# Kernel tuning notes

Hardware: AMD Instinct MI355X
Metric: run time of the kernel (lower is better)

The kernel has to match this reference:

```python
import jax, jax.numpy as jnp
import numpy as np

INF = 1e30
B, L, D_IN, D_STATE, HIDDEN = 32, 4096, 150, 75, 75


def setup_inputs() -> dict:
    key = jax.random.key(0)
    k_in, k_st, k_m, k_w0, k_b0, k_w1, k_b1 = jax.random.split(key, 7)
    inputs = jax.random.normal(k_in, (B, L, D_IN), dtype=jnp.float32)
    state = jax.random.normal(k_st, (B, D_STATE), dtype=jnp.float32)
    c_mask = jax.random.randint(k_m, (B, L), 0, 2).astype(bool)
    # Linear params; torch nn.Linear init scale ~ 1/sqrt(fan_in)
    W0 = jax.random.normal(k_w0, (D_STATE + D_IN, HIDDEN), dtype=jnp.float32) / np.sqrt(D_STATE + D_IN)
    b0 = jax.random.normal(k_b0, (HIDDEN,), dtype=jnp.float32) / np.sqrt(D_STATE + D_IN)
    W1 = jax.random.normal(k_w1, (HIDDEN, 1), dtype=jnp.float32) / np.sqrt(HIDDEN)
    b1 = jax.random.normal(k_b1, (1,), dtype=jnp.float32) / np.sqrt(HIDDEN)
    return {"inputs": inputs, "state": state, "c_mask": c_mask,
            "W0": W0, "b0": b0, "W1": W1, "b1": b1}


def reference(inputs, state, c_mask, W0, b0, W1, b1):
    b, l, _ = inputs.shape
    # u: [B, L, D_STATE + D_IN]  (state broadcast along L, concat with inputs)
    u = jnp.concatenate(
        [jnp.broadcast_to(state[:, None, :], (b, l, state.shape[-1])), inputs],
        axis=2)
    s0 = jnp.tanh(u @ W0 + b0)               # [B, L, HIDDEN]
    s = (s0 @ W1 + b1)[..., 0]               # [B, L]
    s1 = s - INF * (1.0 - c_mask.astype(s.dtype))
    a = jax.nn.softmax(s1, axis=-1)           # [B, L]
    res = jnp.sum(inputs * a[..., None], axis=1, keepdims=True)  # [B, 1, D_IN]
    return res, s1
```

## Files before the change

### kernel.cpp

```cpp
#include <hip/hip_runtime.h>

#define B_    32
#define L_    4096
#define DIN   150
#define DST   75
#define HID   75
#define HPAD  80
#define INF30 1e30f
#define SPART 152


__device__ __forceinline__ float tanh_fast(float p) {
    float e = __expf(-2.f * fabsf(p));
    float t = (1.f - e) / (1.f + e);
    return copysignf(t, p);
}

__global__ __launch_bounds__(256) void k_prep(
    const float* __restrict__ W0, const float* __restrict__ W1,
    float* __restrict__ W0p, float* __restrict__ W1p) {
    int i = blockIdx.x * 256 + threadIdx.x;
    if (i < DIN * HPAD) {
        int d = i / HPAD, h = i - d * HPAD;
        W0p[i] = (h < HID) ? W0[(DST + d) * HID + h] : 0.f;
    }
    if (i < HPAD) W1p[i] = (i < HID) ? W1[i] : 0.f;
}

__global__ __launch_bounds__(128) void k_statepre(
    const float* __restrict__ state, const float* __restrict__ W0,
    const float* __restrict__ b0, float* __restrict__ sp) {
    int b = blockIdx.x;
    int h = threadIdx.x;
    if (h < HPAD) {
        float acc = 0.f;
        if (h < HID) {
            acc = b0[h];
            #pragma unroll 5
            for (int k = 0; k < DST; ++k)
                acc = fmaf(state[b * DST + k], W0[k * HID + h], acc);
        }
        sp[b * HPAD + h] = acc;
    }
}

__global__ __launch_bounds__(256, 4) void k_main(
    const float* __restrict__ in, const unsigned char* __restrict__ maskB,
    const float* __restrict__ W0p, const float* __restrict__ W1p,
    const float* __restrict__ b1, const float* __restrict__ sp,
    float* __restrict__ s1out, float* __restrict__ part) {
    __shared__ __align__(16) float XT[DIN * 64];
    __shared__ __align__(16) float sred2[4 * 64];
    __shared__ __align__(16) float wvals[64];

    int blk = blockIdx.x, tid = threadIdx.x;
    int b = blk >> 6, l0 = (blk & 63) << 6;
    const float4* src4 = (const float4*)(in + (size_t)(b * L_ + l0) * DIN);

    #pragma unroll
    for (int p = 0; p < 10; ++p) {
        int i4 = p * 256 + tid;
        if (i4 < 2400) {
            float4 v = src4[i4];
            int idx = i4 << 2;
            float vals[4] = {v.x, v.y, v.z, v.w};
            #pragma unroll
            for (int e = 0; e < 4; ++e) {
                int id = idx + e;
                int r = id / DIN;
                int k = id - r * DIN;
                XT[(k << 6) + (((r >> 2) ^ (k & 15)) << 2) + (r & 3)] = vals[e];
            }
        }
    }
    __syncthreads();

    int rg = tid & 15, cg = tid >> 4;
    float acc[4][5];
    {
        float s0 = sp[b * HPAD + (cg << 2) + 0];
        float s1_ = sp[b * HPAD + (cg << 2) + 1];
        float s2 = sp[b * HPAD + (cg << 2) + 2];
        float s3 = sp[b * HPAD + (cg << 2) + 3];
        float s4 = sp[b * HPAD + 64 + cg];
        #pragma unroll
        for (int j = 0; j < 4; ++j) {
            acc[j][0] = s0; acc[j][1] = s1_; acc[j][2] = s2;
            acc[j][3] = s3; acc[j][4] = s4;
        }
    }
    const float* wb4 = W0p + (cg << 2);
    const float* wb1 = W0p + 64 + cg;
    #pragma unroll 6
    for (int k = 0; k < DIN; ++k) {
        float4 xv = *(const float4*)&XT[(k << 6) + ((rg ^ (k & 15)) << 2)];
        float4 wv = *(const float4*)&wb4[k * HPAD];
        float  w4 = wb1[k * HPAD];
        float xj[4] = {xv.x, xv.y, xv.z, xv.w};
        #pragma unroll
        for (int j = 0; j < 4; ++j) {
            acc[j][0] = fmaf(xj[j], wv.x, acc[j][0]);
            acc[j][1] = fmaf(xj[j], wv.y, acc[j][1]);
            acc[j][2] = fmaf(xj[j], wv.z, acc[j][2]);
            acc[j][3] = fmaf(xj[j], wv.w, acc[j][3]);
            acc[j][4] = fmaf(xj[j], w4,   acc[j][4]);
        }
    }

    float w1a = W1p[(cg << 2) + 0], w1b = W1p[(cg << 2) + 1];
    float w1c = W1p[(cg << 2) + 2], w1d = W1p[(cg << 2) + 3];
    float w1e = W1p[64 + cg];
    int wv_ = tid >> 6, lane = tid & 63;
    float spart[4];
    #pragma unroll
    for (int j = 0; j < 4; ++j) {
        float s = 0.f;
        s = fmaf(tanh_fast(acc[j][0]), w1a, s);
        s = fmaf(tanh_fast(acc[j][1]), w1b, s);
        s = fmaf(tanh_fast(acc[j][2]), w1c, s);
        s = fmaf(tanh_fast(acc[j][3]), w1d, s);
        s = fmaf(tanh_fast(acc[j][4]), w1e, s);
        s += __shfl_xor(s, 16, 64);
        s += __shfl_xor(s, 32, 64);
        spart[j] = s;
    }
    if (lane < 16) {
        #pragma unroll
        for (int j = 0; j < 4; ++j)
            sred2[(wv_ << 6) + (lane << 2) + j] = spart[j];
    }
    __syncthreads();

    if (tid < 64) {
        float s = b1[0] + sred2[tid] + sred2[64 + tid]
                + sred2[128 + tid] + sred2[192 + tid];
        unsigned char probe = maskB[tid * 4 + 1];
        bool isI32 = __all(probe == 0);
        int l = l0 + tid;
        bool mv = isI32 ? (((const int*)maskB)[b * L_ + l] != 0)
                        : (maskB[b * L_ + l] != 0);
        float s1v = s - (mv ? 0.f : INF30);
        s1out[b * L_ + l] = s1v;
        float mx = s1v;
        #pragma unroll
        for (int off = 1; off < 64; off <<= 1)
            mx = fmaxf(mx, __shfl_xor(mx, off, 64));
        float wexp = __expf(s1v - mx);
        wvals[tid] = wexp;
        float z = wexp;
        #pragma unroll
        for (int off = 1; off < 64; off <<= 1) z += __shfl_xor(z, off, 64);
        if (tid == 0) {
            part[(size_t)blk * SPART + 150] = z;
            part[(size_t)blk * SPART + 151] = mx;
        }
    }
    __syncthreads();

    if (tid < DIN) {
        float t0 = 0.f, t1 = 0.f, t2 = 0.f, t3 = 0.f;
        int dd = tid & 15;
        #pragma unroll
        for (int lq = 0; lq < 16; ++lq) {
            float4 xt = *(const float4*)&XT[(tid << 6) + ((lq ^ dd) << 2)];
            float4 wq = *(const float4*)&wvals[lq << 2];
            t0 = fmaf(xt.x, wq.x, t0);
            t1 = fmaf(xt.y, wq.y, t1);
            t2 = fmaf(xt.z, wq.z, t2);
            t3 = fmaf(xt.w, wq.w, t3);
        }
        part[(size_t)blk * SPART + tid] = (t0 + t1) + (t2 + t3);
    }
}

__global__ __launch_bounds__(192) void k_combine(
    const float* __restrict__ part, float* __restrict__ res) {
    int b = blockIdx.x, tid = threadIdx.x;
    float M = -INFINITY;
    #pragma unroll 8
    for (int c = 0; c < 64; ++c)
        M = fmaxf(M, part[(size_t)((b << 6) + c) * SPART + 151]);
    if (tid < DIN) {
        float ts = 0.f, zs = 0.f;
        #pragma unroll 4
        for (int c = 0; c < 64; ++c) {
            const float* pc = part + (size_t)((b << 6) + c) * SPART;
            float e = __expf(pc[151] - M);
            ts = fmaf(pc[tid], e, ts);
            zs = fmaf(pc[150], e, zs);
        }
        res[b * DIN + tid] = ts / zs;
    }
}

extern "C" void kernel_launch(void* const* d_in, const int* in_sizes, int n_in,
                              void* d_out, int out_size, void* d_ws, size_t ws_size,
                              hipStream_t stream) {
    const float*         inputs = (const float*)d_in[0];
    const float*         state  = (const float*)d_in[1];
    const unsigned char* cmask  = (const unsigned char*)d_in[2];
    const float*         W0     = (const float*)d_in[3];
    const float*         b0     = (const float*)d_in[4];
    const float*         W1     = (const float*)d_in[5];
    const float*         b1     = (const float*)d_in[6];

    float* res  = (float*)d_out;
    float* s1   = (float*)d_out + B_ * DIN;
    float* wsf  = (float*)d_ws;
    float* W0p  = wsf;
    float* W1p  = W0p + DIN * HPAD;
    float* sp   = W1p + HPAD;
    float* part = sp + B_ * HPAD;

    k_prep<<<(DIN * HPAD + 255) / 256, 256, 0, stream>>>(W0, W1, W0p, W1p);
    k_statepre<<<B_, 128, 0, stream>>>(state, W0, b0, sp);
    k_main<<<B_ * L_ / 64, 256, 0, stream>>>(inputs, cmask, W0p, W1p, b1, sp,
                                             s1, part);
    k_combine<<<B_, 192, 0, stream>>>(part, res);
}
```

Measured before the change: 196.4 us.

## Fuse prep kernels and last-block combine, change LDS slot swizzle

Merges the weight-padding and state-projection kernels into one launch. The final softmax combine moves into the main kernel through an atomic per-batch ticket, so the last block of each batch does the reduction. This removes two kernel launches and their inter-kernel gaps. It also replaces the XOR swizzle of the transposed input tile in shared memory with an additive rotating slot pattern, meant to change bank-conflict behaviour, at the cost of extra fences, atomics and a serial tail on one block per batch.

```diff
diff --git a/kernel.cpp b/kernel.cpp
--- a/kernel.cpp
+++ b/kernel.cpp
@@ -18,40 +18,45 @@
 
 __global__ __launch_bounds__(256) void k_prep(
     const float* __restrict__ W0, const float* __restrict__ W1,
-    float* __restrict__ W0p, float* __restrict__ W1p) {
-    int i = blockIdx.x * 256 + threadIdx.x;
-    if (i < DIN * HPAD) {
-        int d = i / HPAD, h = i - d * HPAD;
-        W0p[i] = (h < HID) ? W0[(DST + d) * HID + h] : 0.f;
-    }
-    if (i < HPAD) W1p[i] = (i < HID) ? W1[i] : 0.f;
-}
-
-__global__ __launch_bounds__(128) void k_statepre(
-    const float* __restrict__ state, const float* __restrict__ W0,
-    const float* __restrict__ b0, float* __restrict__ sp) {
-    int b = blockIdx.x;
-    int h = threadIdx.x;
-    if (h < HPAD) {
-        float acc = 0.f;
-        if (h < HID) {
-            acc = b0[h];
-            #pragma unroll 5
-            for (int k = 0; k < DST; ++k)
-                acc = fmaf(state[b * DST + k], W0[k * HID + h], acc);
-        }
-        sp[b * HPAD + h] = acc;
-    }
-}
-
-__global__ __launch_bounds__(256, 4) void k_main(
+    const float* __restrict__ state, const float* __restrict__ b0,
+    float* __restrict__ W0p, float* __restrict__ W1p,
+    float* __restrict__ sp, int* __restrict__ cnt) {
+    int blk = blockIdx.x, tid = threadIdx.x;
+    if (blk < 47) {
+        int i = blk * 256 + tid;
+        if (i < DIN * HPAD) {
+            int d = i / HPAD, h = i - d * HPAD;
+            W0p[i] = (h < HID) ? W0[(DST + d) * HID + h] : 0.f;
+        }
+    } else if (blk == 47) {
+        if (tid < HPAD) W1p[tid] = (tid < HID) ? W1[tid] : 0.f;
+        if (tid >= 128 && tid < 128 + B_) cnt[tid - 128] = 0;
+    } else {
+        int idx = (blk - 48) * 256 + tid;
+        if (idx < B_ * HPAD) {
+            int b = idx / HPAD, h = idx - b * HPAD;
+            float acc = 0.f;
+            if (h < HID) {
+                acc = b0[h];
+                #pragma unroll 5
+                for (int k = 0; k < DST; ++k)
+                    acc = fmaf(state[b * DST + k], W0[k * HID + h], acc);
+            }
+            sp[idx] = acc;
+        }
+    }
+}
+
+__global__ __launch_bounds__(256, 4) void k_fused(
     const float* __restrict__ in, const unsigned char* __restrict__ maskB,
     const float* __restrict__ W0p, const float* __restrict__ W1p,
     const float* __restrict__ b1, const float* __restrict__ sp,
-    float* __restrict__ s1out, float* __restrict__ part) {
+    float* __restrict__ s1out, float* __restrict__ part,
+    int* __restrict__ cnt, float* __restrict__ res) {
     __shared__ __align__(16) float XT[DIN * 64];
-    __shared__ __align__(16) float sred2[4 * 64];
+    __shared__ __align__(16) float sred2[4 * 64 + 2];
     __shared__ __align__(16) float wvals[64];
+    __shared__ int ticket;
 
     int blk = blockIdx.x, tid = threadIdx.x;
     int b = blk >> 6, l0 = (blk & 63) << 6;
@@ -69,7 +74,8 @@
                 int id = idx + e;
                 int r = id / DIN;
                 int k = id - r * DIN;
-                XT[(k << 6) + (((r >> 2) ^ (k & 15)) << 2) + (r & 3)] = vals[e];
+                int slot = ((r >> 2) + k + (k >> 2)) & 15;
+                XT[(k << 6) + (slot << 2) + (r & 3)] = vals[e];
             }
         }
     }
@@ -93,7 +99,8 @@
     const float* wb1 = W0p + 64 + cg;
     #pragma unroll 6
     for (int k = 0; k < DIN; ++k) {
-        float4 xv = *(const float4*)&XT[(k << 6) + ((rg ^ (k & 15)) << 2)];
+        int slot = (rg + k + (k >> 2)) & 15;
+        float4 xv = *(const float4*)&XT[(k << 6) + (slot << 2)];
         float4 wv = *(const float4*)&wb4[k * HPAD];
         float  w4 = wb1[k * HPAD];
         float xj[4] = {xv.x, xv.y, xv.z, xv.w};
@@ -159,10 +166,10 @@
 
     if (tid < DIN) {
         float t0 = 0.f, t1 = 0.f, t2 = 0.f, t3 = 0.f;
-        int dd = tid & 15;
         #pragma unroll
         for (int lq = 0; lq < 16; ++lq) {
-            float4 xt = *(const float4*)&XT[(tid << 6) + ((lq ^ dd) << 2)];
+            int slot = (lq + tid + (tid >> 2)) & 15;
+            float4 xt = *(const float4*)&XT[(tid << 6) + (slot << 2)];
             float4 wq = *(const float4*)&wvals[lq << 2];
             t0 = fmaf(xt.x, wq.x, t0);
             t1 = fmaf(xt.y, wq.y, t1);
@@ -171,25 +178,38 @@
         }
         part[(size_t)blk * SPART + tid] = (t0 + t1) + (t2 + t3);
     }
-}
-
-__global__ __launch_bounds__(192) void k_combine(
-    const float* __restrict__ part, float* __restrict__ res) {
-    int b = blockIdx.x, tid = threadIdx.x;
-    float M = -INFINITY;
-    #pragma unroll 8
-    for (int c = 0; c < 64; ++c)
-        M = fmaxf(M, part[(size_t)((b << 6) + c) * SPART + 151]);
+
+    __syncthreads();
+    if (tid == 0) {
+        __threadfence();
+        ticket = atomicAdd(&cnt[b], 1);
+    }
+    __syncthreads();
+    if (ticket != 63) return;
+    __threadfence();
+
+    const float* pb = part + (size_t)(b << 6) * SPART;
+    if (tid < 64) {
+        float mc = pb[(size_t)tid * SPART + 151];
+        float mm = mc;
+        #pragma unroll
+        for (int off = 1; off < 64; off <<= 1)
+            mm = fmaxf(mm, __shfl_xor(mm, off, 64));
+        float e = __expf(mc - mm);
+        sred2[tid] = e;
+        float zp = pb[(size_t)tid * SPART + 150] * e;
+        #pragma unroll
+        for (int off = 1; off < 64; off <<= 1) zp += __shfl_xor(zp, off, 64);
+        if (tid == 0) sred2[256] = zp;
+    }
+    __syncthreads();
     if (tid < DIN) {
-        float ts = 0.f, zs = 0.f;
-        #pragma unroll 4
-        for (int c = 0; c < 64; ++c) {
-            const float* pc = part + (size_t)((b << 6) + c) * SPART;
-            float e = __expf(pc[151] - M);
-            ts = fmaf(pc[tid], e, ts);
-            zs = fmaf(pc[150], e, zs);
-        }
-        res[b * DIN + tid] = ts / zs;
+        float Z = sred2[256];
+        float ts = 0.f;
+        #pragma unroll 8
+        for (int c = 0; c < 64; ++c)
+            ts = fmaf(pb[(size_t)c * SPART + tid], sred2[c], ts);
+        res[b * DIN + tid] = ts / Z;
     }
 }
 
@@ -211,10 +231,9 @@
     float* W1p  = W0p + DIN * HPAD;
     float* sp   = W1p + HPAD;
     float* part = sp + B_ * HPAD;
-
-    k_prep<<<(DIN * HPAD + 255) / 256, 256, 0, stream>>>(W0, W1, W0p, W1p);
-    k_statepre<<<B_, 128, 0, stream>>>(state, W0, b0, sp);
-    k_main<<<B_ * L_ / 64, 256, 0, stream>>>(inputs, cmask, W0p, W1p, b1, sp,
-                                             s1, part);
-    k_combine<<<B_, 192, 0, stream>>>(part, res);
-}
+    int*   cnt  = (int*)(part + 2048 * SPART);
+
+    k_prep<<<58, 256, 0, stream>>>(W0, W1, state, b0, W0p, W1p, sp, cnt);
+    k_fused<<<B_ * L_ / 64, 256, 0, stream>>>(inputs, cmask, W0p, W1p, b1, sp,
+                                              s1, part, cnt, res);
+}
```

Measured after the change: 252.6 us. +28.6%, slower.
